# Optimization experiments

Hardware: AMD Instinct MI355X
Metric: run time of the kernel (lower is better)

## Reference

```python
import jax, jax.numpy as jnp
import numpy as np

N_NODES = 1_000_000
N_EDGES = 16_000_000


def setup_inputs() -> dict:
    key = jax.random.key(0)
    ks = jax.random.split(key, 12)
    feat = jax.random.normal(ks[0], (N_NODES, 1), dtype=jnp.float32)
    # symmetric GCN norm D^{-1/2}; positive values in (0, 1]
    norm = jax.random.uniform(ks[1], (N_NODES, 1), dtype=jnp.float32, minval=0.05, maxval=1.0)
    src = jax.random.randint(ks[2], (N_EDGES,), 0, N_NODES, dtype=jnp.int32)
    dst = jax.random.randint(ks[3], (N_EDGES,), 0, N_NODES, dtype=jnp.int32)
    dims = [(1, 3), (3, 3), (3, 3), (3, 3), (3, 3), (3, 1)]
    params = {}
    for i, (fi, fo) in enumerate(dims):
        w = jax.random.normal(ks[4 + i], (fi, fo), dtype=jnp.float32) * (1.0 / np.sqrt(fi))
        params[f"W{i+1}"] = w
        params[f"b{i+1}"] = jnp.zeros((fo,), dtype=jnp.float32)
    return dict(feat=feat, norm=norm, src=src, dst=dst, **params)


def _gcn_layer(h, norm, W, b, src, dst, n_nodes):
    # DGL-style GraphConv with symmetric norm:
    #   h = h * norm; agg_i = sum_{(j->i) in E} h_j; h = agg * norm; h = h @ W + b; relu
    h = h * norm                                   # [N, F]
    msgs = jnp.take(h, src, axis=0)                # [E, F] irregular gather
    agg = jax.ops.segment_sum(msgs, dst, num_segments=n_nodes)  # [N, F] scatter-add
    agg = agg * norm
    return jax.nn.relu(agg @ W + b)


def reference(feat, norm, W1, b1, W2, b2, W3, b3, W4, b4, W5, b5, W6, b6, src, dst):
    n = feat.shape[0]
    h = feat
    for W, b in ((W1, b1), (W2, b2), (W3, b3), (W4, b4), (W5, b5), (W6, b6)):
        h = _gcn_layer(h, norm, W, b, src, dst, n)
    return h  # [N, 1]
```

## Files before the change

kernel.cpp:

```cpp
#include <hip/hip_runtime.h>


#define BT 256
#define NBLK 256
#define BSHIFT 11
#define BSIZE 2048
#define LMASK 2047
#define SSH 18
#define NBINS 2048
#define M (NBLK * NBINS)
#define BTL 1024

__device__ __forceinline__ int edge_key(int s, int d) {
  return ((d >> BSHIFT) << 2) | (s >> SSH);
}

__global__ void k_init(const float* __restrict__ feat, const float* __restrict__ norm,
                       float* __restrict__ s0, int N) {
  int i = blockIdx.x * BT + threadIdx.x;
  if (i < N) s0[i] = feat[i] * norm[i];
}

__global__ void k_phist(const int* __restrict__ src, const int* __restrict__ dst,
                        int* __restrict__ histB, int E, int chunk) {
  __shared__ int h[NBINS];
  for (int i = threadIdx.x; i < NBINS; i += BT) h[i] = 0;
  __syncthreads();
  int b = blockIdx.x;
  int beg = b * chunk, end = min(beg + chunk, E);
  int i = beg + (int)threadIdx.x * 4;
  for (; i + 3 < end; i += BT * 4) {
    int4 u = *(const int4*)(src + i);
    int4 v = *(const int4*)(dst + i);
    atomicAdd(&h[edge_key(u.x, v.x)], 1);
    atomicAdd(&h[edge_key(u.y, v.y)], 1);
    atomicAdd(&h[edge_key(u.z, v.z)], 1);
    atomicAdd(&h[edge_key(u.w, v.w)], 1);
  }
  for (; i < end; ++i) atomicAdd(&h[edge_key(src[i], dst[i])], 1);
  __syncthreads();
  for (int k = threadIdx.x; k < NBINS; k += BT) histB[b * NBINS + k] = h[k];
}

__global__ void k_transp(const int* __restrict__ in, int* __restrict__ out, int R, int C) {
  __shared__ int tile[64][65];
  int c0 = blockIdx.x * 64, r0 = blockIdx.y * 64;
  int tx = threadIdx.x & 63, ty = threadIdx.x >> 6;
  for (int j = 0; j < 16; ++j) {
    int r = ty + j * 4;
    tile[r][tx] = in[(r0 + r) * C + c0 + tx];
  }
  __syncthreads();
  for (int j = 0; j < 16; ++j) {
    int r = ty + j * 4;
    out[(c0 + r) * R + r0 + tx] = tile[tx][r];
  }
}

__global__ void k_blockSum(const int* __restrict__ data, int* __restrict__ partial, int Mlen) {
  __shared__ int tmp[BT];
  int i = blockIdx.x * BT + threadIdx.x;
  tmp[threadIdx.x] = (i < Mlen) ? data[i] : 0;
  __syncthreads();
  for (int off = BT / 2; off > 0; off >>= 1) {
    if (threadIdx.x < off) tmp[threadIdx.x] += tmp[threadIdx.x + off];
    __syncthreads();
  }
  if (threadIdx.x == 0) partial[blockIdx.x] = tmp[0];
}

__global__ void k_scanPartials(int* __restrict__ partial, int nb) {
  __shared__ int tmp[BT];
  __shared__ int carry;
  int t = threadIdx.x;
  if (t == 0) carry = 0;
  __syncthreads();
  for (int base = 0; base < nb; base += BT) {
    int i = base + t;
    int v = (i < nb) ? partial[i] : 0;
    tmp[t] = v;
    __syncthreads();
    for (int off = 1; off < BT; off <<= 1) {
      int x = 0;
      if (t >= off) x = tmp[t - off];
      __syncthreads();
      tmp[t] += x;
      __syncthreads();
    }
    if (i < nb) partial[i] = tmp[t] - v + carry;
    __syncthreads();
    if (t == BT - 1) carry += tmp[BT - 1];
    __syncthreads();
  }
}

__global__ void k_scanFinal(int* __restrict__ data, const int* __restrict__ partial, int Mlen) {
  __shared__ int tmp[BT];
  int t = threadIdx.x;
  int i = blockIdx.x * BT + t;
  int v = (i < Mlen) ? data[i] : 0;
  tmp[t] = v;
  __syncthreads();
  for (int off = 1; off < BT; off <<= 1) {
    int x = 0;
    if (t >= off) x = tmp[t - off];
    __syncthreads();
    tmp[t] += x;
    __syncthreads();
  }
  if (i < Mlen) data[i] = tmp[t] - v + partial[blockIdx.x];
}

__global__ void k_pscatter(const int* __restrict__ src, const int* __restrict__ dst,
                           const int* __restrict__ scanT, unsigned int* __restrict__ packed,
                           int E, int chunk) {
  __shared__ int cur[NBINS];
  int b = blockIdx.x;
  for (int k = threadIdx.x; k < NBINS; k += BT) cur[k] = scanT[b * NBINS + k];
  __syncthreads();
  int beg = b * chunk, end = min(beg + chunk, E);
  int i = beg + (int)threadIdx.x * 4;
  for (; i + 3 < end; i += BT * 4) {
    int4 u = *(const int4*)(src + i);
    int4 v = *(const int4*)(dst + i);
    int p;
    p = atomicAdd(&cur[edge_key(u.x, v.x)], 1);
    packed[p] = ((unsigned)u.x << BSHIFT) | (unsigned)(v.x & LMASK);
    p = atomicAdd(&cur[edge_key(u.y, v.y)], 1);
    packed[p] = ((unsigned)u.y << BSHIFT) | (unsigned)(v.y & LMASK);
    p = atomicAdd(&cur[edge_key(u.z, v.z)], 1);
    packed[p] = ((unsigned)u.z << BSHIFT) | (unsigned)(v.z & LMASK);
    p = atomicAdd(&cur[edge_key(u.w, v.w)], 1);
    packed[p] = ((unsigned)u.w << BSHIFT) | (unsigned)(v.w & LMASK);
  }
  for (; i < end; ++i) {
    int p = atomicAdd(&cur[edge_key(src[i], dst[i])], 1);
    packed[p] = ((unsigned)src[i] << BSHIFT) | (unsigned)(dst[i] & LMASK);
  }
}


#define ACC3(p)                                             \
  {                                                         \
    unsigned pp = (p);                                      \
    float4 m = ((const float4*)sPrev)[pp >> BSHIFT];        \
    int loc = pp & LMASK;                                   \
    atomicAdd(&a0[loc], m.x);                               \
    atomicAdd(&a1[loc], m.y);                               \
    atomicAdd(&a2[loc], m.z);                               \
  }

#define ACC1(p)                                             \
  {                                                         \
    unsigned pp = (p);                                      \
    atomicAdd(&a[pp & LMASK], sIn[pp >> BSHIFT]);           \
  }

#define GATH4(m, p) float4 m = ((const float4*)sPrev)[(p) >> BSHIFT];
#define ATOM3(m, p)                                         \
  {                                                         \
    int loc = (int)((p) & LMASK);                           \
    atomicAdd(&a0[loc], m.x);                               \
    atomicAdd(&a1[loc], m.y);                               \
    atomicAdd(&a2[loc], m.z);                               \
  }
#define GATH1(m, p) float m = sIn[(p) >> BSHIFT];
#define ATOM1(m, p) atomicAdd(&a[(p) & LMASK], m);

#define EDGE_LOOP3                                          \
  int abeg = min(end, (beg + 3) & ~3);                      \
  int t = beg + (int)threadIdx.x;                           \
  if (t < abeg) ACC3(packed[t]);                            \
  int i = abeg + (int)threadIdx.x * 8;                      \
  for (; i + 7 < end; i += BTL * 8) {                       \
    uint4 pa = *(const uint4*)(packed + i);                 \
    uint4 pb = *(const uint4*)(packed + i + 4);             \
    GATH4(m0, pa.x) GATH4(m1, pa.y)                         \
    GATH4(m2, pa.z) GATH4(m3, pa.w)                         \
    GATH4(m4, pb.x) GATH4(m5, pb.y)                         \
    GATH4(m6, pb.z) GATH4(m7, pb.w)                         \
    ATOM3(m0, pa.x) ATOM3(m1, pa.y)                         \
    ATOM3(m2, pa.z) ATOM3(m3, pa.w)                         \
    ATOM3(m4, pb.x) ATOM3(m5, pb.y)                         \
    ATOM3(m6, pb.z) ATOM3(m7, pb.w)                         \
  }                                                         \
  for (; i < end; ++i) ACC3(packed[i]);

#define EDGE_LOOP1                                          \
  int abeg = min(end, (beg + 3) & ~3);                      \
  int t = beg + (int)threadIdx.x;                           \
  if (t < abeg) ACC1(packed[t]);                            \
  int i = abeg + (int)threadIdx.x * 8;                      \
  for (; i + 7 < end; i += BTL * 8) {                       \
    uint4 pa = *(const uint4*)(packed + i);                 \
    uint4 pb = *(const uint4*)(packed + i + 4);             \
    GATH1(m0, pa.x) GATH1(m1, pa.y)                         \
    GATH1(m2, pa.z) GATH1(m3, pa.w)                         \
    GATH1(m4, pb.x) GATH1(m5, pb.y)                         \
    GATH1(m6, pb.z) GATH1(m7, pb.w)                         \
    ATOM1(m0, pa.x) ATOM1(m1, pa.y)                         \
    ATOM1(m2, pa.z) ATOM1(m3, pa.w)                         \
    ATOM1(m4, pb.x) ATOM1(m5, pb.y)                         \
    ATOM1(m6, pb.z) ATOM1(m7, pb.w)                         \
  }                                                         \
  for (; i < end; ++i) ACC1(packed[i]);

__global__ __launch_bounds__(BTL, 8) void k_layer1(
    const int* __restrict__ scanT, const unsigned int* __restrict__ packed,
    const float* __restrict__ sIn, const float* __restrict__ norm,
    const float* __restrict__ W1, const float* __restrict__ b1,
    float* __restrict__ sNext, int N) {
  __shared__ float a[BSIZE];
  int k = blockIdx.x;
  for (int ii = threadIdx.x; ii < BSIZE; ii += BTL) a[ii] = 0.0f;
  int beg = scanT[k << 2], end = scanT[(k << 2) + 4];
  __syncthreads();
  EDGE_LOOP1
  __syncthreads();
  int node0 = k << BSHIFT;
  for (int tt = threadIdx.x; tt < BSIZE; tt += BTL) {
    int node = node0 + tt;
    if (node >= N) break;
    float n = norm[node];
    float pre = a[tt] * n;
    float h0 = fmaxf(0.0f, pre * W1[0] + b1[0]);
    float h1 = fmaxf(0.0f, pre * W1[1] + b1[1]);
    float h2 = fmaxf(0.0f, pre * W1[2] + b1[2]);
    ((float4*)sNext)[node] = make_float4(h0 * n, h1 * n, h2 * n, 0.0f);
  }
}

__global__ __launch_bounds__(BTL, 8) void k_layer3(
    const int* __restrict__ scanT, const unsigned int* __restrict__ packed,
    const float* __restrict__ sPrev, const float* __restrict__ norm,
    const float* __restrict__ W, const float* __restrict__ bias,
    float* __restrict__ sNext, int N) {
  __shared__ float a0[BSIZE], a1[BSIZE], a2[BSIZE];
  int k = blockIdx.x;
  for (int ii = threadIdx.x; ii < BSIZE; ii += BTL) { a0[ii] = 0.0f; a1[ii] = 0.0f; a2[ii] = 0.0f; }
  int beg = scanT[k << 2], end = scanT[(k << 2) + 4];
  __syncthreads();
  EDGE_LOOP3
  __syncthreads();
  int node0 = k << BSHIFT;
  for (int tt = threadIdx.x; tt < BSIZE; tt += BTL) {
    int node = node0 + tt;
    if (node >= N) break;
    float n = norm[node];
    float x0 = a0[tt] * n, x1 = a1[tt] * n, x2 = a2[tt] * n;
    float h0 = fmaxf(0.0f, x0 * W[0] + x1 * W[3] + x2 * W[6] + bias[0]);
    float h1 = fmaxf(0.0f, x0 * W[1] + x1 * W[4] + x2 * W[7] + bias[1]);
    float h2 = fmaxf(0.0f, x0 * W[2] + x1 * W[5] + x2 * W[8] + bias[2]);
    ((float4*)sNext)[node] = make_float4(h0 * n, h1 * n, h2 * n, 0.0f);
  }
}

__global__ __launch_bounds__(BTL, 8) void k_layer5(
    const int* __restrict__ scanT, const unsigned int* __restrict__ packed,
    const float* __restrict__ sPrev, const float* __restrict__ norm,
    const float* __restrict__ W5, const float* __restrict__ b5,
    const float* __restrict__ W6, float* __restrict__ sB, int N) {
  __shared__ float a0[BSIZE], a1[BSIZE], a2[BSIZE];
  int k = blockIdx.x;
  for (int ii = threadIdx.x; ii < BSIZE; ii += BTL) { a0[ii] = 0.0f; a1[ii] = 0.0f; a2[ii] = 0.0f; }
  int beg = scanT[k << 2], end = scanT[(k << 2) + 4];
  __syncthreads();
  EDGE_LOOP3
  __syncthreads();
  int node0 = k << BSHIFT;
  for (int tt = threadIdx.x; tt < BSIZE; tt += BTL) {
    int node = node0 + tt;
    if (node >= N) break;
    float n = norm[node];
    float x0 = a0[tt] * n, x1 = a1[tt] * n, x2 = a2[tt] * n;
    float h0 = fmaxf(0.0f, x0 * W5[0] + x1 * W5[3] + x2 * W5[6] + b5[0]);
    float h1 = fmaxf(0.0f, x0 * W5[1] + x1 * W5[4] + x2 * W5[7] + b5[1]);
    float h2 = fmaxf(0.0f, x0 * W5[2] + x1 * W5[5] + x2 * W5[8] + b5[2]);
    sB[node] = (h0 * W6[0] + h1 * W6[1] + h2 * W6[2]) * n;
  }
}

__global__ __launch_bounds__(BTL, 8) void k_layer6(
    const int* __restrict__ scanT, const unsigned int* __restrict__ packed,
    const float* __restrict__ sIn, const float* __restrict__ norm,
    const float* __restrict__ b6, float* __restrict__ out, int N) {
  __shared__ float a[BSIZE];
  int k = blockIdx.x;
  for (int ii = threadIdx.x; ii < BSIZE; ii += BTL) a[ii] = 0.0f;
  int beg = scanT[k << 2], end = scanT[(k << 2) + 4];
  __syncthreads();
  EDGE_LOOP1
  __syncthreads();
  int node0 = k << BSHIFT;
  for (int tt = threadIdx.x; tt < BSIZE; tt += BTL) {
    int node = node0 + tt;
    if (node >= N) break;
    out[node] = fmaxf(0.0f, a[tt] * norm[node] + b6[0]);
  }
}

extern "C" void kernel_launch(void* const* d_in, const int* in_sizes, int n_in,
                              void* d_out, int out_size, void* d_ws, size_t ws_size,
                              hipStream_t stream) {
  const float* feat = (const float*)d_in[0];
  const float* norm = (const float*)d_in[1];
  const int* src = (const int*)d_in[2];
  const int* dst = (const int*)d_in[3];
  const float* W1 = (const float*)d_in[4];
  const float* b1 = (const float*)d_in[5];
  const float* W2 = (const float*)d_in[6];
  const float* b2 = (const float*)d_in[7];
  const float* W3 = (const float*)d_in[8];
  const float* b3 = (const float*)d_in[9];
  const float* W4 = (const float*)d_in[10];
  const float* b4 = (const float*)d_in[11];
  const float* W5 = (const float*)d_in[12];
  const float* b5 = (const float*)d_in[13];
  const float* W6 = (const float*)d_in[14];
  const float* b6 = (const float*)d_in[15];
  float* out = (float*)d_out;

  const int N = in_sizes[0];
  const int E = in_sizes[2];
  const int nbNode = (N + BT - 1) / BT;
  const int nBkt = (N + BSIZE - 1) >> BSHIFT;
  const int chunk = (((E + NBLK - 1) / NBLK) + 3) & ~3;

  unsigned int* packed = (unsigned int*)d_ws;
  int* scanT = (int*)(packed + (size_t)E);
  int* partial = scanT + (size_t)M;
  float* s0B = (float*)(partial + M / BT);
  float* sA = s0B + (size_t)N;
  float* sA2 = sA + (size_t)4 * N;
  int* histB = (int*)sA;
  int* histT = histB + (size_t)M;

  k_init<<<nbNode, BT, 0, stream>>>(feat, norm, s0B, N);
  k_phist<<<NBLK, BT, 0, stream>>>(src, dst, histB, E, chunk);
  {
    dim3 g1(NBINS / 64, NBLK / 64);
    k_transp<<<g1, BT, 0, stream>>>(histB, histT, NBLK, NBINS);
  }
  k_blockSum<<<M / BT, BT, 0, stream>>>(histT, partial, M);
  k_scanPartials<<<1, BT, 0, stream>>>(partial, M / BT);
  k_scanFinal<<<M / BT, BT, 0, stream>>>(histT, partial, M);
  {
    dim3 g2(NBLK / 64, NBINS / 64);
    k_transp<<<g2, BT, 0, stream>>>(histT, scanT, NBINS, NBLK);
  }
  k_pscatter<<<NBLK, BT, 0, stream>>>(src, dst, scanT, packed, E, chunk);

  k_layer1<<<nBkt, BTL, 0, stream>>>(scanT, packed, s0B, norm, W1, b1, sA, N);
  k_layer3<<<nBkt, BTL, 0, stream>>>(scanT, packed, sA, norm, W2, b2, sA2, N);
  k_layer3<<<nBkt, BTL, 0, stream>>>(scanT, packed, sA2, norm, W3, b3, sA, N);
  k_layer3<<<nBkt, BTL, 0, stream>>>(scanT, packed, sA, norm, W4, b4, sA2, N);
  k_layer5<<<nBkt, BTL, 0, stream>>>(scanT, packed, sA2, norm, W5, b5, W6, s0B, N);
  k_layer6<<<nBkt, BTL, 0, stream>>>(scanT, packed, s0B, norm, b6, out, N);
}
```

Before: 1.597 ms.

## Software-pipeline packed-edge loads with inline asm and halve layer block size

Rewrites the per-layer edge aggregation loops to prefetch the next iteration's packed edge words while the current iteration's gathers and LDS atomics run. Each thread now handles 12 edges per step, using inline-asm dwordx4 and dword loads with explicit vmcnt waits and scheduling barriers. The layer kernels also drop from 1024 to 512 threads per block, with launch bounds adjusted to match. The aim is to hide gather latency behind more memory requests in flight. In exchange, register pressure rises, and the full vmcnt(0) waits also stall on the prefetch loads.

```diff
diff --git a/kernel.cpp b/kernel.cpp
--- a/kernel.cpp
+++ b/kernel.cpp
@@ -9,7 +9,10 @@
 #define SSH 18
 #define NBINS 2048
 #define M (NBLK * NBINS)
-#define BTL 1024
+#define BTL 512
+
+typedef float __attribute__((ext_vector_type(4))) f32x4;
+typedef unsigned int __attribute__((ext_vector_type(4))) u32x4;
 
 __device__ __forceinline__ int edge_key(int s, int d) {
   return ((d >> BSHIFT) << 2) | (s >> SSH);
@@ -140,6 +143,17 @@
 }
 
 
+#define PKLOAD(d, idx) \
+  asm volatile("global_load_dwordx4 %0, %1, off" : "=v"(d) : "v"(packed + (idx)))
+#define G4A(md, pw) \
+  asm volatile("global_load_dwordx4 %0, %1, off" \
+               : "=v"(md) : "v"((const f32x4*)sPrev + ((pw) >> BSHIFT)))
+#define G1A(md, pw) \
+  asm volatile("global_load_dword %0, %1, off" \
+               : "=v"(md) : "v"(sIn + ((pw) >> BSHIFT)))
+#define VMCNT0 asm volatile("s_waitcnt vmcnt(0)" ::: "memory")
+#define SCHED0 __builtin_amdgcn_sched_barrier(0)
+
 #define ACC3(p)                                             \
   {                                                         \
     unsigned pp = (p);                                      \
@@ -156,7 +170,6 @@
     atomicAdd(&a[pp & LMASK], sIn[pp >> BSHIFT]);           \
   }
 
-#define GATH4(m, p) float4 m = ((const float4*)sPrev)[(p) >> BSHIFT];
 #define ATOM3(m, p)                                         \
   {                                                         \
     int loc = (int)((p) & LMASK);                           \
@@ -164,48 +177,65 @@
     atomicAdd(&a1[loc], m.y);                               \
     atomicAdd(&a2[loc], m.z);                               \
   }
-#define GATH1(m, p) float m = sIn[(p) >> BSHIFT];
 #define ATOM1(m, p) atomicAdd(&a[(p) & LMASK], m);
 
-#define EDGE_LOOP3                                          \
-  int abeg = min(end, (beg + 3) & ~3);                      \
-  int t = beg + (int)threadIdx.x;                           \
-  if (t < abeg) ACC3(packed[t]);                            \
-  int i = abeg + (int)threadIdx.x * 8;                      \
-  for (; i + 7 < end; i += BTL * 8) {                       \
-    uint4 pa = *(const uint4*)(packed + i);                 \
-    uint4 pb = *(const uint4*)(packed + i + 4);             \
-    GATH4(m0, pa.x) GATH4(m1, pa.y)                         \
-    GATH4(m2, pa.z) GATH4(m3, pa.w)                         \
-    GATH4(m4, pb.x) GATH4(m5, pb.y)                         \
-    GATH4(m6, pb.z) GATH4(m7, pb.w)                         \
-    ATOM3(m0, pa.x) ATOM3(m1, pa.y)                         \
-    ATOM3(m2, pa.z) ATOM3(m3, pa.w)                         \
-    ATOM3(m4, pb.x) ATOM3(m5, pb.y)                         \
-    ATOM3(m6, pb.z) ATOM3(m7, pb.w)                         \
-  }                                                         \
+#define EDGE_LOOP3                                                        \
+  int abeg = min(end, (beg + 3) & ~3);                                    \
+  { int t0 = beg + (int)threadIdx.x; if (t0 < abeg) ACC3(packed[t0]); }   \
+  int i = abeg + (int)threadIdx.x * 12;                                   \
+  if (i + 11 < end) {                                                     \
+    u32x4 c0, c1, c2;                                                     \
+    PKLOAD(c0, i); PKLOAD(c1, i + 4); PKLOAD(c2, i + 8);                  \
+    VMCNT0; SCHED0;                                                       \
+    for (;;) {                                                            \
+      int j = i + BTL * 12;                                               \
+      bool more = (j + 11 < end);                                         \
+      u32x4 n0, n1, n2;                                                   \
+      if (more) { PKLOAD(n0, j); PKLOAD(n1, j + 4); PKLOAD(n2, j + 8); }  \
+      f32x4 m0, m1, m2, m3, m4, m5, m6, m7, m8, m9, ma, mb;               \
+      G4A(m0, c0.x); G4A(m1, c0.y); G4A(m2, c0.z); G4A(m3, c0.w);         \
+      G4A(m4, c1.x); G4A(m5, c1.y); G4A(m6, c1.z); G4A(m7, c1.w);         \
+      G4A(m8, c2.x); G4A(m9, c2.y); G4A(ma, c2.z); G4A(mb, c2.w);         \
+      VMCNT0; SCHED0;                                                     \
+      ATOM3(m0, c0.x) ATOM3(m1, c0.y) ATOM3(m2, c0.z) ATOM3(m3, c0.w)     \
+      ATOM3(m4, c1.x) ATOM3(m5, c1.y) ATOM3(m6, c1.z) ATOM3(m7, c1.w)     \
+      ATOM3(m8, c2.x) ATOM3(m9, c2.y) ATOM3(ma, c2.z) ATOM3(mb, c2.w)     \
+      i = j;                                                              \
+      if (!more) break;                                                   \
+      c0 = n0; c1 = n1; c2 = n2;                                          \
+    }                                                                     \
+  }                                                                       \
   for (; i < end; ++i) ACC3(packed[i]);
 
-#define EDGE_LOOP1                                          \
-  int abeg = min(end, (beg + 3) & ~3);                      \
-  int t = beg + (int)threadIdx.x;                           \
-  if (t < abeg) ACC1(packed[t]);                            \
-  int i = abeg + (int)threadIdx.x * 8;                      \
-  for (; i + 7 < end; i += BTL * 8) {                       \
-    uint4 pa = *(const uint4*)(packed + i);                 \
-    uint4 pb = *(const uint4*)(packed + i + 4);             \
-    GATH1(m0, pa.x) GATH1(m1, pa.y)                         \
-    GATH1(m2, pa.z) GATH1(m3, pa.w)                         \
-    GATH1(m4, pb.x) GATH1(m5, pb.y)                         \
-    GATH1(m6, pb.z) GATH1(m7, pb.w)                         \
-    ATOM1(m0, pa.x) ATOM1(m1, pa.y)                         \
-    ATOM1(m2, pa.z) ATOM1(m3, pa.w)                         \
-    ATOM1(m4, pb.x) ATOM1(m5, pb.y)                         \
-    ATOM1(m6, pb.z) ATOM1(m7, pb.w)                         \
-  }                                                         \
+#define EDGE_LOOP1                                                        \
+  int abeg = min(end, (beg + 3) & ~3);                                    \
+  { int t0 = beg + (int)threadIdx.x; if (t0 < abeg) ACC1(packed[t0]); }   \
+  int i = abeg + (int)threadIdx.x * 12;                                   \
+  if (i + 11 < end) {                                                     \
+    u32x4 c0, c1, c2;                                                     \
+    PKLOAD(c0, i); PKLOAD(c1, i + 4); PKLOAD(c2, i + 8);                  \
+    VMCNT0; SCHED0;                                                       \
+    for (;;) {                                                            \
+      int j = i + BTL * 12;                                               \
+      bool more = (j + 11 < end);                                         \
+      u32x4 n0, n1, n2;                                                   \
+      if (more) { PKLOAD(n0, j); PKLOAD(n1, j + 4); PKLOAD(n2, j + 8); }  \
+      float m0, m1, m2, m3, m4, m5, m6, m7, m8, m9, ma, mb;               \
+      G1A(m0, c0.x); G1A(m1, c0.y); G1A(m2, c0.z); G1A(m3, c0.w);         \
+      G1A(m4, c1.x); G1A(m5, c1.y); G1A(m6, c1.z); G1A(m7, c1.w);         \
+      G1A(m8, c2.x); G1A(m9, c2.y); G1A(ma, c2.z); G1A(mb, c2.w);         \
+      VMCNT0; SCHED0;                                                     \
+      ATOM1(m0, c0.x) ATOM1(m1, c0.y) ATOM1(m2, c0.z) ATOM1(m3, c0.w)     \
+      ATOM1(m4, c1.x) ATOM1(m5, c1.y) ATOM1(m6, c1.z) ATOM1(m7, c1.w)     \
+      ATOM1(m8, c2.x) ATOM1(m9, c2.y) ATOM1(ma, c2.z) ATOM1(mb, c2.w)     \
+      i = j;                                                              \
+      if (!more) break;                                                   \
+      c0 = n0; c1 = n1; c2 = n2;                                          \
+    }                                                                     \
+  }                                                                       \
   for (; i < end; ++i) ACC1(packed[i]);
 
-__global__ __launch_bounds__(BTL, 8) void k_layer1(
+__global__ __launch_bounds__(BTL, 4) void k_layer1(
     const int* __restrict__ scanT, const unsigned int* __restrict__ packed,
     const float* __restrict__ sIn, const float* __restrict__ norm,
     const float* __restrict__ W1, const float* __restrict__ b1,
@@ -230,7 +260,7 @@
   }
 }
 
-__global__ __launch_bounds__(BTL, 8) void k_layer3(
+__global__ __launch_bounds__(BTL, 4) void k_layer3(
     const int* __restrict__ scanT, const unsigned int* __restrict__ packed,
     const float* __restrict__ sPrev, const float* __restrict__ norm,
     const float* __restrict__ W, const float* __restrict__ bias,
@@ -255,7 +285,7 @@
   }
 }
 
-__global__ __launch_bounds__(BTL, 8) void k_layer5(
+__global__ __launch_bounds__(BTL, 4) void k_layer5(
     const int* __restrict__ scanT, const unsigned int* __restrict__ packed,
     const float* __restrict__ sPrev, const float* __restrict__ norm,
     const float* __restrict__ W5, const float* __restrict__ b5,
@@ -280,7 +310,7 @@
   }
 }
 
-__global__ __launch_bounds__(BTL, 8) void k_layer6(
+__global__ __launch_bounds__(BTL, 4) void k_layer6(
     const int* __restrict__ scanT, const unsigned int* __restrict__ packed,
     const float* __restrict__ sIn, const float* __restrict__ norm,
     const float* __restrict__ b6, float* __restrict__ out, int N) {
```

Result: no change. 1.607 ms (+0.7%).
